# Optimization experiments

Measured on AMD Instinct MI355X. Metric: run time of the kernel, lower is better.

The kernel has to match this reference:

```python
import jax, jax.numpy as jnp
import numpy as np

N_NODES = 100000
N_EDGES = 1600000
D_IN, D_EMB, D_POOL = 256, 128, 64
EPS = 1e-6


def setup_inputs() -> dict:
    key = jax.random.key(0)
    ks = jax.random.split(key, 10)
    x = jax.random.normal(ks[0], (N_NODES, D_IN), dtype=jnp.float32)
    edge_src = jax.random.randint(ks[1], (N_EDGES,), 0, N_NODES, dtype=jnp.int32)
    edge_dst = jax.random.randint(ks[2], (N_EDGES,), 0, N_NODES, dtype=jnp.int32)
    edge_weight = jax.random.uniform(ks[3], (N_EDGES,), dtype=jnp.float32)
    # glorot-ish init for the three GraphConvolution weights
    w1 = jax.random.normal(ks[4], (D_IN, D_EMB), dtype=jnp.float32) / np.sqrt(D_IN)
    b1 = jnp.zeros((D_EMB,), dtype=jnp.float32)
    wp = jax.random.normal(ks[5], (D_EMB, D_POOL), dtype=jnp.float32) / np.sqrt(D_EMB)
    bp = jnp.zeros((D_POOL,), dtype=jnp.float32)
    w2 = jax.random.normal(ks[6], (D_EMB, D_POOL), dtype=jnp.float32) / np.sqrt(D_EMB)
    b2 = jnp.zeros((D_POOL,), dtype=jnp.float32)
    return {"x": x, "edge_src": edge_src, "edge_dst": edge_dst,
            "edge_weight": edge_weight, "w1": w1, "b1": b1,
            "wp": wp, "bp": bp, "w2": w2, "b2": b2}


def _gcn(h, w, b, edge_src, edge_dst, edge_weight, n_nodes):
    # GraphConvolution: support = h @ w ; out = adj @ support + b (sparse spmm)
    support = h @ w                                  # [N, d_out]
    msgs = edge_weight[:, None] * support[edge_src]  # [E, d_out] gather
    agg = jax.ops.segment_sum(msgs, edge_dst, num_segments=n_nodes)
    return agg + b


def _pairnorm_si(h):
    # PairNorm mode 'PN-SI' (scale=1): center over nodes, row-wise L2 normalize
    h = h - jnp.mean(h, axis=0, keepdims=True)
    rownorm = jnp.sqrt(EPS + jnp.sum(h * h, axis=1, keepdims=True))
    return h / rownorm


def reference(x, edge_src, edge_dst, edge_weight, w1, b1, wp, bp, w2, b2):
    n = x.shape[0]
    enc1 = _gcn(x, w1, b1, edge_src, edge_dst, edge_weight, n)
    enc1 = jax.nn.relu(_pairnorm_si(enc1))
    pool1 = _gcn(enc1, wp, bp, edge_src, edge_dst, edge_weight, n)
    pool1 = jax.nn.softmax(_pairnorm_si(pool1), axis=-1)
    enc2 = _gcn(enc1, w2, b2, edge_src, edge_dst, edge_weight, n)
    enc2 = jax.nn.relu(_pairnorm_si(enc2))
    return enc2, pool1
```

## Files before the change

### kernel.cpp

```cpp
#include <hip/hip_runtime.h>
#include <stdint.h>

#define N_NODES 100000
#define N_EDGES 1600000
#define N_SCAN_BLOCKS ((N_NODES + 1023) / 1024)
#define N_SLICES 128
#define SLICE_E (N_EDGES / N_SLICES)

typedef __attribute__((ext_vector_type(8))) short bf16x8;
typedef __attribute__((ext_vector_type(4))) float f32x4;

__device__ __forceinline__ uint32_t f2bf(float f) {
  uint32_t u = __float_as_uint(f);
  u += 0x7fffu + ((u >> 16) & 1);
  return u >> 16;
}
__device__ __forceinline__ float bf_lo(uint32_t v) { return __uint_as_float(v << 16); }
__device__ __forceinline__ float bf_hi(uint32_t v) { return __uint_as_float(v & 0xffff0000u); }
__device__ __forceinline__ uint32_t pack2(float a, float b) { return f2bf(a) | (f2bf(b) << 16); }

__global__ void k_hist(const int* __restrict__ dst, int* __restrict__ deg) {
  int e = blockIdx.x * 256 + threadIdx.x;
  if (e < N_EDGES) atomicAdd(&deg[dst[e]], 1);
}

__global__ __launch_bounds__(256) void k_scan_local(const int* __restrict__ deg,
                                                    int* __restrict__ row_ptr,
                                                    int* __restrict__ blocksum) {
  __shared__ int lds[256];
  int base = blockIdx.x * 1024 + threadIdx.x * 4;
  int v0 = (base     < N_NODES) ? deg[base]     : 0;
  int v1 = (base + 1 < N_NODES) ? deg[base + 1] : 0;
  int v2 = (base + 2 < N_NODES) ? deg[base + 2] : 0;
  int v3 = (base + 3 < N_NODES) ? deg[base + 3] : 0;
  int tsum = v0 + v1 + v2 + v3;
  lds[threadIdx.x] = tsum;
  __syncthreads();
  for (int off = 1; off < 256; off <<= 1) {
    int t = (threadIdx.x >= (unsigned)off) ? lds[threadIdx.x - off] : 0;
    __syncthreads();
    lds[threadIdx.x] += t;
    __syncthreads();
  }
  int run = lds[threadIdx.x] - tsum;
  if (base     < N_NODES) row_ptr[base]     = run;            run += v0;
  if (base + 1 < N_NODES) row_ptr[base + 1] = run;            run += v1;
  if (base + 2 < N_NODES) row_ptr[base + 2] = run;            run += v2;
  if (base + 3 < N_NODES) row_ptr[base + 3] = run;
  if (threadIdx.x == 255) blocksum[blockIdx.x] = lds[255];
}

__global__ __launch_bounds__(128) void k_scan_blocks(int* __restrict__ blocksum) {
  __shared__ int lds[128];
  int v = (threadIdx.x < N_SCAN_BLOCKS) ? blocksum[threadIdx.x] : 0;
  lds[threadIdx.x] = v;
  __syncthreads();
  for (int off = 1; off < 128; off <<= 1) {
    int t = (threadIdx.x >= (unsigned)off) ? lds[threadIdx.x - off] : 0;
    __syncthreads();
    lds[threadIdx.x] += t;
    __syncthreads();
  }
  if (threadIdx.x < N_SCAN_BLOCKS) blocksum[threadIdx.x] = lds[threadIdx.x] - v;
}

__global__ __launch_bounds__(256) void k_scan_add(int* __restrict__ row_ptr,
                                                  const int* __restrict__ blocksum) {
  int i = blockIdx.x * 256 + threadIdx.x;
  if (i < N_NODES) row_ptr[i] += blocksum[i >> 10];
  if (i == 0) row_ptr[N_NODES] = N_EDGES;
}

__global__ __launch_bounds__(256) void k_scatter(const int* __restrict__ src,
                                                 const int* __restrict__ dst,
                                                 const float* __restrict__ w,
                                                 const int* __restrict__ row_ptr,
                                                 int* __restrict__ fill,
                                                 int2* __restrict__ rec) {
  unsigned rng = blockIdx.x & 7;
  int base = (blockIdx.x >> 3) * SLICE_E;
  for (int it = 0; it < (SLICE_E + 255) / 256; ++it) {
    int e = base + it * 256 + threadIdx.x;
    if (e < base + SLICE_E) {
      int d = dst[e];
      if (__umulhi((unsigned)d, 343598u) == rng) {
        int pos = row_ptr[d] + atomicAdd(&fill[d], 1);
        rec[pos] = make_int2(src[e], __float_as_int(w[e]));
      }
    }
  }
}

__global__ void k_pack(const float* __restrict__ w1, const float* __restrict__ wp,
                       const float* __restrict__ w2, uint16_t* __restrict__ wT1,
                       uint16_t* __restrict__ wTc) {
  int i = blockIdx.x * 256 + threadIdx.x;
  if (i < 128 * 256) {
    int n = i >> 8, k = i & 255;
    wT1[n * 256 + (k ^ ((n & 7) << 3))] = (uint16_t)f2bf(w1[k * 128 + n]);
  }
  int j = i - 128 * 256;
  if (j >= 0 && j < 128 * 128) {
    int n = j >> 7, k = j & 127;
    wTc[n * 128 + (k ^ ((n & 7) << 3))] =
        (uint16_t)f2bf((n < 64) ? wp[k * 64 + n] : w2[k * 64 + (n - 64)]);
  }
}

__global__ __launch_bounds__(256) void k_gemm1(const float* __restrict__ A,
                                               const uint16_t* __restrict__ wTs,
                                               uint16_t* __restrict__ C, int M) {
  __shared__ uint16_t bs[128 * 256];
  {
    const float4* s = (const float4*)wTs;
    float4* d = (float4*)bs;
#pragma unroll
    for (int i = 0; i < 16; i++) d[i * 256 + threadIdx.x] = s[i * 256 + threadIdx.x];
  }
  __syncthreads();

  int wave = threadIdx.x >> 6, lane = threadIdx.x & 63;
  int m0 = (blockIdx.x * 4 + wave) * 16;
  int quad = lane >> 4, mcol = lane & 15;
  int xsw = (mcol & 7) << 3;
  int arow = m0 + mcol;
  bool av = arow < M;

  float4 abuf[16];
  const float* ap = A + (size_t)arow * 256 + quad * 8;
  if (av) {
#pragma unroll
    for (int t = 0; t < 8; t++) {
      abuf[2 * t]     = *(const float4*)(ap + t * 32);
      abuf[2 * t + 1] = *(const float4*)(ap + t * 32 + 4);
    }
  } else {
#pragma unroll
    for (int t = 0; t < 16; t++) abuf[t] = (float4){0.f, 0.f, 0.f, 0.f};
  }

  const uint16_t* bp = bs + mcol * 256;

  f32x4 acc[8];
#pragma unroll
  for (int nt = 0; nt < 8; nt++) acc[nt] = (f32x4){0.f, 0.f, 0.f, 0.f};

#pragma unroll
  for (int it = 0; it < 8; it++) {
    float4 lo = abuf[2 * it], hi = abuf[2 * it + 1];
    bf16x8 a;
    a[0] = (short)f2bf(lo.x); a[1] = (short)f2bf(lo.y);
    a[2] = (short)f2bf(lo.z); a[3] = (short)f2bf(lo.w);
    a[4] = (short)f2bf(hi.x); a[5] = (short)f2bf(hi.y);
    a[6] = (short)f2bf(hi.z); a[7] = (short)f2bf(hi.w);
#pragma unroll
    for (int nt = 0; nt < 8; nt++) {
      bf16x8 b = *(const bf16x8*)(bp + nt * 4096 + ((it * 32 + quad * 8) ^ xsw));
      acc[nt] = __builtin_amdgcn_mfma_f32_16x16x32_bf16(a, b, acc[nt], 0, 0, 0);
    }
  }
#pragma unroll
  for (int r = 0; r < 4; r++) {
    int row = m0 + quad * 4 + r;
    if (row < M) {
#pragma unroll
      for (int nt = 0; nt < 8; nt++)
        C[(size_t)row * 128 + nt * 16 + mcol] = (uint16_t)f2bf(acc[nt][r]);
    }
  }
}

__global__ __launch_bounds__(256) void k_gemm2(const uint16_t* __restrict__ A,
                                               const uint16_t* __restrict__ wTs,
                                               uint16_t* __restrict__ C, int M) {
  __shared__ uint16_t bs[128 * 128];
  {
    const float4* s = (const float4*)wTs;
    float4* d = (float4*)bs;
#pragma unroll
    for (int i = 0; i < 8; i++) d[i * 256 + threadIdx.x] = s[i * 256 + threadIdx.x];
  }
  __syncthreads();

  int wave = threadIdx.x >> 6, lane = threadIdx.x & 63;
  int m0 = (blockIdx.x * 4 + wave) * 16;
  int quad = lane >> 4, mcol = lane & 15;
  int xsw = (mcol & 7) << 3;
  int arow = m0 + mcol;
  bool av = arow < M;

  bf16x8 abuf[4];
  const uint16_t* ap = A + (size_t)arow * 128 + quad * 8;
  if (av) {
#pragma unroll
    for (int t = 0; t < 4; t++) abuf[t] = *(const bf16x8*)(ap + t * 32);
  } else {
#pragma unroll
    for (int t = 0; t < 4; t++) abuf[t] = (bf16x8){};
  }

  const uint16_t* bp = bs + mcol * 128;

  f32x4 acc[8];
#pragma unroll
  for (int nt = 0; nt < 8; nt++) acc[nt] = (f32x4){0.f, 0.f, 0.f, 0.f};

#pragma unroll
  for (int it = 0; it < 4; it++) {
#pragma unroll
    for (int nt = 0; nt < 8; nt++) {
      bf16x8 b = *(const bf16x8*)(bp + nt * 2048 + ((it * 32 + quad * 8) ^ xsw));
      acc[nt] = __builtin_amdgcn_mfma_f32_16x16x32_bf16(abuf[it], b, acc[nt], 0, 0, 0);
    }
  }
#pragma unroll
  for (int r = 0; r < 4; r++) {
    int row = m0 + quad * 4 + r;
    if (row < M) {
#pragma unroll
      for (int nt = 0; nt < 8; nt++)
        C[(size_t)row * 128 + nt * 16 + mcol] = (uint16_t)f2bf(acc[nt][r]);
    }
  }
}

__global__ __launch_bounds__(256) void k_spmm(const uint16_t* __restrict__ sup,
                                              const int* __restrict__ row_ptr,
                                              const int2* __restrict__ rec,
                                              uint16_t* __restrict__ agg) {
  int row = blockIdx.x * 4 + (threadIdx.x >> 6);
  if (row >= N_NODES) return;
  int lane = threadIdx.x & 63;
  int s = row_ptr[row], e = row_ptr[row + 1];
  float a0 = 0.f, a1 = 0.f;
  int i = s;
  for (; i + 8 <= e; i += 8) {
    int2 r[8];
    uint32_t v[8];
#pragma unroll
    for (int u = 0; u < 8; u++) r[u] = rec[i + u];
#pragma unroll
    for (int u = 0; u < 8; u++)
      v[u] = *(const uint32_t*)(sup + (size_t)r[u].x * 128 + lane * 2);
#pragma unroll
    for (int u = 0; u < 8; u++) {
      float w = __int_as_float(r[u].y);
      a0 += w * bf_lo(v[u]);
      a1 += w * bf_hi(v[u]);
    }
  }
  for (; i < e; i++) {
    int2 r = rec[i];
    uint32_t v = *(const uint32_t*)(sup + (size_t)r.x * 128 + lane * 2);
    float w = __int_as_float(r.y);
    a0 += w * bf_lo(v);
    a1 += w * bf_hi(v);
  }
  *(uint32_t*)(agg + (size_t)row * 128 + lane * 2) = pack2(a0, a1);
}

__global__ __launch_bounds__(256) void k_colsum(const uint16_t* __restrict__ agg,
                                                float* __restrict__ cs) {
  __shared__ float sd[256];
  int col = threadIdx.x & 127, half = threadIdx.x >> 7;
  int r0 = blockIdx.x * 256;
  float local = 0.f;
  for (int r = r0 + half; r < r0 + 256 && r < N_NODES; r += 2)
    local += __uint_as_float(((uint32_t)agg[(size_t)r * 128 + col]) << 16);
  sd[threadIdx.x] = local;
  __syncthreads();
  if (threadIdx.x < 128) atomicAdd(&cs[col], sd[threadIdx.x] + sd[threadIdx.x + 128]);
}

__global__ __launch_bounds__(256) void k_pn1(uint16_t* __restrict__ agg,
                                             const float* __restrict__ cs) {
  int row = blockIdx.x * 4 + (threadIdx.x >> 6);
  if (row >= N_NODES) return;
  int lane = threadIdx.x & 63;
  const float invn = 1.0f / (float)N_NODES;
  uint32_t v = *(const uint32_t*)(agg + (size_t)row * 128 + lane * 2);
  float h0 = bf_lo(v) - cs[lane * 2] * invn;
  float h1 = bf_hi(v) - cs[lane * 2 + 1] * invn;
  float ss = h0 * h0 + h1 * h1;
#pragma unroll
  for (int m = 1; m < 64; m <<= 1) ss += __shfl_xor(ss, m, 64);
  float rinv = rsqrtf(1e-6f + ss);
  *(uint32_t*)(agg + (size_t)row * 128 + lane * 2) =
      pack2(fmaxf(h0 * rinv, 0.f), fmaxf(h1 * rinv, 0.f));
}

__global__ __launch_bounds__(256) void k_final(const uint16_t* __restrict__ agg,
                                               const float* __restrict__ cs,
                                               float* __restrict__ out) {
  int row = blockIdx.x * 4 + (threadIdx.x >> 6);
  if (row >= N_NODES) return;
  int lane = threadIdx.x & 63;
  const float invn = 1.0f / (float)N_NODES;
  uint32_t v = *(const uint32_t*)(agg + (size_t)row * 128 + lane * 2);
  float h0 = bf_lo(v) - cs[lane * 2] * invn;
  float h1 = bf_hi(v) - cs[lane * 2 + 1] * invn;
  float ss = h0 * h0 + h1 * h1;
#pragma unroll
  for (int m = 1; m < 32; m <<= 1) ss += __shfl_xor(ss, m, 64);
  float rinv = rsqrtf(1e-6f + ss);
  float p0 = h0 * rinv, p1 = h1 * rinv;
  if (lane < 32) {
    float mx = fmaxf(p0, p1);
#pragma unroll
    for (int m = 1; m < 32; m <<= 1) mx = fmaxf(mx, __shfl_xor(mx, m, 64));
    float e0 = __expf(p0 - mx), e1 = __expf(p1 - mx);
    float sum = e0 + e1;
#pragma unroll
    for (int m = 1; m < 32; m <<= 1) sum += __shfl_xor(sum, m, 64);
    float inv = 1.0f / sum;
    float2 o = {e0 * inv, e1 * inv};
    *(float2*)(out + (size_t)N_NODES * 64 + (size_t)row * 64 + lane * 2) = o;
  } else {
    int l = lane - 32;
    float2 o = {fmaxf(p0, 0.f), fmaxf(p1, 0.f)};
    *(float2*)(out + (size_t)row * 64 + l * 2) = o;
  }
}

extern "C" void kernel_launch(void* const* d_in, const int* in_sizes, int n_in,
                              void* d_out, int out_size, void* d_ws, size_t ws_size,
                              hipStream_t stream) {
  const float* x    = (const float*)d_in[0];
  const int*   esrc = (const int*)d_in[1];
  const int*   edst = (const int*)d_in[2];
  const float* ew   = (const float*)d_in[3];
  const float* w1   = (const float*)d_in[4];
  const float* wp   = (const float*)d_in[6];
  const float* w2   = (const float*)d_in[8];
  float* out = (float*)d_out;

  char* ws = (char*)d_ws;
  size_t off = 0;
  auto alloc = [&](size_t bytes) {
    char* p = ws + off;
    off += (bytes + 255) & ~(size_t)255;
    return p;
  };
  uint16_t* support = (uint16_t*)alloc((size_t)N_NODES * 128 * 2);
  uint16_t* agg     = (uint16_t*)alloc((size_t)N_NODES * 128 * 2);
  int2*     rec     = (int2*)alloc((size_t)N_EDGES * 8);
  int*      row_ptr = (int*)alloc((size_t)(N_NODES + 1) * 4);
  int*      bsum    = (int*)alloc((size_t)N_SCAN_BLOCKS * 4);
  size_t zero_start = off;
  int*      deg     = (int*)alloc((size_t)N_NODES * 4);
  int*      fill    = (int*)alloc((size_t)N_NODES * 4);
  float*    cs      = (float*)alloc(256 * 4);
  size_t zero_bytes = off - zero_start;
  uint16_t* wT1     = (uint16_t*)alloc(128 * 256 * 2);
  uint16_t* wTc     = (uint16_t*)alloc(128 * 128 * 2);
  (void)ws_size; (void)in_sizes; (void)n_in; (void)out_size;

  hipMemsetAsync(deg, 0, zero_bytes, stream);

  k_hist<<<(N_EDGES + 255) / 256, 256, 0, stream>>>(edst, deg);
  k_scan_local<<<N_SCAN_BLOCKS, 256, 0, stream>>>(deg, row_ptr, bsum);
  k_scan_blocks<<<1, 128, 0, stream>>>(bsum);
  k_scan_add<<<(N_NODES + 255) / 256, 256, 0, stream>>>(row_ptr, bsum);
  k_scatter<<<8 * N_SLICES, 256, 0, stream>>>(esrc, edst, ew, row_ptr, fill, rec);
  k_pack<<<192, 256, 0, stream>>>(w1, wp, w2, wT1, wTc);

  k_gemm1<<<(N_NODES + 63) / 64, 256, 0, stream>>>(x, wT1, support, N_NODES);
  k_spmm<<<(N_NODES + 3) / 4, 256, 0, stream>>>(support, row_ptr, rec, agg);
  k_colsum<<<(N_NODES + 255) / 256, 256, 0, stream>>>(agg, cs);
  k_pn1<<<(N_NODES + 3) / 4, 256, 0, stream>>>(agg, cs);

  k_gemm2<<<(N_NODES + 63) / 64, 256, 0, stream>>>(agg, wTc, support, N_NODES);
  k_spmm<<<(N_NODES + 3) / 4, 256, 0, stream>>>(support, row_ptr, rec, agg);
  k_colsum<<<(N_NODES + 255) / 256, 256, 0, stream>>>(agg, cs + 128);
  k_final<<<(N_NODES + 3) / 4, 256, 0, stream>>>(agg, cs + 128, out);
}
```

Before: 627.5 us.

## Build CSR edge records with a two-level LDS bucket sort

Replaces the edge scatter kernel, which re-read the destination array eight times and placed each record with a global atomic and a random write, with a bucket sort on dst>>10. The new pipeline has four kernels: per-block bucket histograms, a single-block exclusive scan, a scatter that stages records per bucket in LDS before coalesced flushes, and a per-bucket fill that orders records by node in LDS before writing them contiguously. The aim is to cut redundant reads and scattered global atomics and writes in CSR construction. In exchange it adds kernel launches and a serial single-block scan, and it reuses the support buffer as scratch space.

```diff
diff --git a/kernel.cpp b/kernel.cpp
--- a/kernel.cpp
+++ b/kernel.cpp
@@ -4,8 +4,13 @@
 #define N_NODES 100000
 #define N_EDGES 1600000
 #define N_SCAN_BLOCKS ((N_NODES + 1023) / 1024)
-#define N_SLICES 128
-#define SLICE_E (N_EDGES / N_SLICES)
+
+#define NBKT 98
+#define NBLK_A 250
+#define SLICE_A 6400
+#define NCNT (NBKT * NBLK_A)
+#define BCAP 112
+#define RCAP 17280
 
 typedef __attribute__((ext_vector_type(8))) short bf16x8;
 typedef __attribute__((ext_vector_type(4))) float f32x4;
@@ -71,22 +76,103 @@
   if (i == 0) row_ptr[N_NODES] = N_EDGES;
 }
 
-__global__ __launch_bounds__(256) void k_scatter(const int* __restrict__ src,
-                                                 const int* __restrict__ dst,
-                                                 const float* __restrict__ w,
-                                                 const int* __restrict__ row_ptr,
-                                                 int* __restrict__ fill,
-                                                 int2* __restrict__ rec) {
-  unsigned rng = blockIdx.x & 7;
-  int base = (blockIdx.x >> 3) * SLICE_E;
-  for (int it = 0; it < (SLICE_E + 255) / 256; ++it) {
+
+__global__ __launch_bounds__(256) void k_bh(const int* __restrict__ dst,
+                                            int* __restrict__ cnt) {
+  __shared__ int lc[NBKT];
+  for (int k = threadIdx.x; k < NBKT; k += 256) lc[k] = 0;
+  __syncthreads();
+  int base = blockIdx.x * SLICE_A;
+#pragma unroll
+  for (int it = 0; it < SLICE_A / 256; ++it)
+    atomicAdd(&lc[dst[base + it * 256 + threadIdx.x] >> 10], 1);
+  __syncthreads();
+  for (int k = threadIdx.x; k < NBKT; k += 256) cnt[k * NBLK_A + blockIdx.x] = lc[k];
+}
+
+__global__ __launch_bounds__(1024) void k_bscan(int* __restrict__ cnt) {
+  __shared__ int part[1024];
+  const int C = (NCNT + 1023) / 1024;
+  int b0 = threadIdx.x * C;
+  int s = 0;
+#pragma unroll
+  for (int j = 0; j < C; ++j) { int i = b0 + j; if (i < NCNT) s += cnt[i]; }
+  part[threadIdx.x] = s;
+  __syncthreads();
+  for (int off = 1; off < 1024; off <<= 1) {
+    int t = (threadIdx.x >= (unsigned)off) ? part[threadIdx.x - off] : 0;
+    __syncthreads();
+    part[threadIdx.x] += t;
+    __syncthreads();
+  }
+  int run = part[threadIdx.x] - s;
+  for (int j = 0; j < C; ++j) {
+    int i = b0 + j;
+    if (i < NCNT) { int v = cnt[i]; cnt[i] = run; run += v; }
+  }
+}
+
+__global__ __launch_bounds__(256) void k_bscatter(const int* __restrict__ src,
+                                                  const int* __restrict__ dst,
+                                                  const float* __restrict__ w,
+                                                  const int* __restrict__ cnt,
+                                                  int2* __restrict__ esw,
+                                                  int* __restrict__ ed) {
+  __shared__ int2 ssw[NBKT][BCAP];
+  __shared__ int  sd[NBKT][BCAP];
+  __shared__ int  ofs0[NBKT], lcnt[NBKT];
+  for (int k = threadIdx.x; k < NBKT; k += 256) {
+    ofs0[k] = cnt[k * NBLK_A + blockIdx.x];
+    lcnt[k] = 0;
+  }
+  __syncthreads();
+  int base = blockIdx.x * SLICE_A;
+#pragma unroll 1
+  for (int it = 0; it < SLICE_A / 256; ++it) {
     int e = base + it * 256 + threadIdx.x;
-    if (e < base + SLICE_E) {
-      int d = dst[e];
-      if (__umulhi((unsigned)d, 343598u) == rng) {
-        int pos = row_ptr[d] + atomicAdd(&fill[d], 1);
-        rec[pos] = make_int2(src[e], __float_as_int(w[e]));
-      }
+    int d = dst[e];
+    int bkt = d >> 10;
+    int r = atomicAdd(&lcnt[bkt], 1);
+    int2 sw = make_int2(src[e], __float_as_int(w[e]));
+    if (r < BCAP) { ssw[bkt][r] = sw; sd[bkt][r] = d; }
+    else { esw[ofs0[bkt] + r] = sw; ed[ofs0[bkt] + r] = d; }
+  }
+  __syncthreads();
+  int wave = threadIdx.x >> 6, lane = threadIdx.x & 63;
+  for (int k = wave; k < NBKT; k += 4) {
+    int n = lcnt[k] < BCAP ? lcnt[k] : BCAP;
+    int o = ofs0[k];
+    for (int j = lane; j < n; j += 64) { esw[o + j] = ssw[k][j]; ed[o + j] = sd[k][j]; }
+  }
+}
+
+__global__ __launch_bounds__(256) void k_bfill(const int2* __restrict__ esw,
+                                               const int* __restrict__ ed,
+                                               const int* __restrict__ row_ptr,
+                                               int2* __restrict__ rec) {
+  __shared__ int2 stg[RCAP];
+  __shared__ int lrp[1025];
+  __shared__ int lfl[1024];
+  int n0 = blockIdx.x << 10;
+  int nn = (N_NODES - n0 < 1024) ? (N_NODES - n0) : 1024;
+  for (int k = threadIdx.x; k <= nn; k += 256) lrp[k] = row_ptr[n0 + k];
+  for (int k = threadIdx.x; k < nn; k += 256) lfl[k] = 0;
+  __syncthreads();
+  int base = lrp[0];
+  int cntb = lrp[nn] - base;
+  if (cntb <= RCAP) {
+    for (int i = threadIdx.x; i < cntb; i += 256) {
+      int li = ed[base + i] - n0;
+      int p = lrp[li] - base + atomicAdd(&lfl[li], 1);
+      stg[p] = esw[base + i];
+    }
+    __syncthreads();
+    for (int i = threadIdx.x; i < cntb; i += 256) rec[base + i] = stg[i];
+  } else {
+    for (int i = threadIdx.x; i < cntb; i += 256) {
+      int li = ed[base + i] - n0;
+      int p = lrp[li] + atomicAdd(&lfl[li], 1);
+      rec[p] = esw[base + i];
     }
   }
 }
@@ -346,13 +432,15 @@
   int2*     rec     = (int2*)alloc((size_t)N_EDGES * 8);
   int*      row_ptr = (int*)alloc((size_t)(N_NODES + 1) * 4);
   int*      bsum    = (int*)alloc((size_t)N_SCAN_BLOCKS * 4);
+  int*      cnt     = (int*)alloc((size_t)NCNT * 4);
   size_t zero_start = off;
   int*      deg     = (int*)alloc((size_t)N_NODES * 4);
-  int*      fill    = (int*)alloc((size_t)N_NODES * 4);
   float*    cs      = (float*)alloc(256 * 4);
   size_t zero_bytes = off - zero_start;
   uint16_t* wT1     = (uint16_t*)alloc(128 * 256 * 2);
   uint16_t* wTc     = (uint16_t*)alloc(128 * 128 * 2);
+  int2*     esw     = (int2*)support;
+  int*      ed      = (int*)((char*)support + (size_t)N_EDGES * 8);
   (void)ws_size; (void)in_sizes; (void)n_in; (void)out_size;
 
   hipMemsetAsync(deg, 0, zero_bytes, stream);
@@ -361,7 +449,12 @@
   k_scan_local<<<N_SCAN_BLOCKS, 256, 0, stream>>>(deg, row_ptr, bsum);
   k_scan_blocks<<<1, 128, 0, stream>>>(bsum);
   k_scan_add<<<(N_NODES + 255) / 256, 256, 0, stream>>>(row_ptr, bsum);
-  k_scatter<<<8 * N_SLICES, 256, 0, stream>>>(esrc, edst, ew, row_ptr, fill, rec);
+
+  k_bh<<<NBLK_A, 256, 0, stream>>>(edst, cnt);
+  k_bscan<<<1, 1024, 0, stream>>>(cnt);
+  k_bscatter<<<NBLK_A, 256, 0, stream>>>(esrc, edst, ew, cnt, esw, ed);
+  k_bfill<<<NBKT, 256, 0, stream>>>(esw, ed, row_ptr, rec);
+
   k_pack<<<192, 256, 0, stream>>>(w1, wp, w2, wT1, wTc);
 
   k_gemm1<<<(N_NODES + 63) / 64, 256, 0, stream>>>(x, wT1, support, N_NODES);
```

Measured after the change: 647.7 us. 3.2% more time.
